# Kernel tuning notes

Measured on AMD Instinct MI355X. Metric: run time of the kernel, lower is better.

## Reference

```python
import jax, jax.numpy as jnp
import numpy as np
import math

B, C_IN, C_QK, H, W, NH = 1, 256, 128, 96, 96, 8
SCALE = math.sqrt(C_QK / NH)  # sqrt(planes/num_head) = 4.0
TEMP = 1.0


def conv1x1(x, w, b=None):
    # x: [B, Cin, H, W], w: [Cout, Cin] -> [B, Cout, H, W]
    y = jnp.einsum('bchw,oc->bohw', x, w)
    if b is not None:
        y = y + b[None, :, None, None]
    return y


def maxpool2x2(x):
    return jax.lax.reduce_window(x, -jnp.inf, jax.lax.max,
                                 (1, 1, 2, 2), (1, 1, 2, 2), 'VALID')


def setup_inputs() -> dict:
    key = jax.random.key(0)
    ks = jax.random.split(key, 5)
    x = jax.random.normal(ks[0], (B, C_IN, H, W), dtype=jnp.float32)
    # conv weights: init.normal_(w, 0, 0.01), zero bias; conv_value has no bias
    w_q = jax.random.normal(ks[1], (C_QK, C_IN), dtype=jnp.float32) * 0.01
    b_q = jnp.zeros((C_QK,), dtype=jnp.float32)
    w_k = jax.random.normal(ks[2], (C_QK, C_IN), dtype=jnp.float32) * 0.01
    b_k = jnp.zeros((C_QK,), dtype=jnp.float32)
    w_v = jax.random.normal(ks[3], (C_IN, C_IN), dtype=jnp.float32) * 0.01
    return {'x': x, 'w_q': w_q, 'b_q': b_q, 'w_k': w_k, 'b_k': b_k, 'w_v': w_v}


def reference(x, w_q, b_q, w_k, b_k, w_v):
    residual = x
    input_x = maxpool2x2(x)                       # [B, Cin, H/2, W/2]
    Hd, Wd = H // 2, W // 2
    Nq, Nk = H * W, Hd * Wd

    q = conv1x1(x, w_q, b_q)                      # [B, Cqk, H, W]
    k = conv1x1(input_x, w_k, b_k)                # [B, Cqk, Hd, Wd]
    v = conv1x1(input_x, w_v)                     # [B, Cin, Hd, Wd]

    dq = C_QK // NH
    dv = C_IN // NH
    q = q.reshape(B * NH, dq, Nq)
    k = k.reshape(B * NH, dq, Nk)
    v = v.reshape(B * NH, dv, Nk)

    # dot distance: scaled by sqrt(planes/num_head) and temp (nowd empty)
    sim = jnp.einsum('bdq,bdk->bqk', q, k) / (SCALE * TEMP)
    attn = jax.nn.softmax(sim, axis=2)            # softmax over keys

    # out = value @ attn^T  -> [B*NH, dv, Nq]
    out = jnp.einsum('bdk,bqk->bdq', v, attn)
    out = out.reshape(B, C_IN, H, W)
    return out + residual
```

## Files before the change

### kernel.cpp

```cpp
#include <hip/hip_runtime.h>
#include <hip/hip_bf16.h>
#include <math.h>

#define C_IN   256
#define C_QK   128
#define NH     8
#define H_     96
#define W_     96
#define NQ     (H_*W_)
#define HD     48
#define WD     48
#define NK     (HD*WD)
#define DQ     16
#define DV     32
#define NQC    (NQ/32)
#define NKC    (NK/32)
#define QPAIRS (NQC/2)
#define KQRT   (NKC/4)
#define KSTEPS (C_IN/16)
#define QS     0.3606737602222409f

typedef __attribute__((ext_vector_type(8)))  short short8v;
typedef __attribute__((ext_vector_type(16))) float f32x16;
typedef __attribute__((ext_vector_type(2)))  int   v2i;

union B8u { uint u[4]; short8v v; };

static __device__ inline ushort bf16r(float f) {
    __hip_bfloat16 h = __float2bfloat16(f);
    return *reinterpret_cast<ushort*>(&h);
}
static __device__ inline uint cvtpk(float lo, float hi) {
    uint r;
    asm("v_cvt_pk_bf16_f32 %0, %1, %2" : "=v"(r) : "v"(lo), "v"(hi));
    return r;
}
static __device__ inline void lswap(uint a, uint b, uint& x, uint& y, int hi) {
#if __has_builtin(__builtin_amdgcn_permlane32_swap)
    v2i r = __builtin_amdgcn_permlane32_swap((int)a, (int)b, false, false);
    x = (uint)r.x;
    y = (uint)r.y;
#else
    uint bx = (uint)__shfl_xor((int)b, 32);
    uint ax = (uint)__shfl_xor((int)a, 32);
    x = hi ? bx : a;
    y = hi ? b : ax;
#endif
}
static __device__ inline float fexp2(float v) {
#if __has_builtin(__builtin_amdgcn_exp2f)
    return __builtin_amdgcn_exp2f(v);
#else
    return __expf(v * 0.6931471805599453f);
#endif
}

#define U_XPB  (NKC*KSTEPS*64)
#define U_WQ   (4*KSTEPS*64)
#define U_WK   (4*KSTEPS*64)
#define U_WV   (8*KSTEPS*64)
#define U_FRAG (U_XPB+U_WQ+U_WK+U_WV)
#define U_TOT  (U_FRAG + 128)

__global__ __launch_bounds__(256) void prep_kernel(
    const float* __restrict__ x,  const float* __restrict__ wq, const float* __restrict__ bq,
    const float* __restrict__ wk, const float* __restrict__ wv,
    ushort* __restrict__ xpbP,
    ushort* __restrict__ wqP, ushort* __restrict__ wkP, ushort* __restrict__ wvP,
    float* __restrict__ bqs)
{
    int t = blockIdx.x * 256 + threadIdx.x;
    if (t >= U_TOT) return;
    if (t >= U_FRAG) { int i = t - U_FRAG; bqs[i] = bq[i] * QS; return; }

    union { ushort s[8]; uint4 v; } ou;
    int u = t;
    if (u < U_XPB) {
        int l = u & 63, rest = u >> 6;
        int ks = rest & 15, nc = rest >> 4;
        int np = nc * 32 + (l & 31);
        int k0 = ks * 16 + 8 * (l >> 5);
        int py = np / WD, px = np - py * WD;
        const float* base = x + (2 * py) * W_ + 2 * px;
        #pragma unroll
        for (int j = 0; j < 8; ++j) {
            const float* p = base + (size_t)(k0 + j) * NQ;
            ou.s[j] = bf16r(fmaxf(fmaxf(p[0], p[1]), fmaxf(p[W_], p[W_ + 1])));
        }
        *(uint4*)&xpbP[(size_t)u * 8] = ou.v;
        return;
    }
    u -= U_XPB;
    if (u < U_WQ) {
        int l = u & 63, ks = (u >> 6) & 15, mb = u >> 10;
        int m = mb * 32 + (l & 31), k0 = ks * 16 + 8 * (l >> 5);
        #pragma unroll
        for (int j = 0; j < 8; ++j) ou.s[j] = bf16r(wq[m * C_IN + k0 + j] * QS);
        *(uint4*)&wqP[(size_t)u * 8] = ou.v;
        return;
    }
    u -= U_WQ;
    if (u < U_WK) {
        int l = u & 63, ks = (u >> 6) & 15, mb = u >> 10;
        int m = mb * 32 + (l & 31), k0 = ks * 16 + 8 * (l >> 5);
        #pragma unroll
        for (int j = 0; j < 8; ++j) ou.s[j] = bf16r(wk[m * C_IN + k0 + j]);
        *(uint4*)&wkP[(size_t)u * 8] = ou.v;
        return;
    }
    u -= U_WK;
    {
        int l = u & 63, ks = (u >> 6) & 15, cb = u >> 10;
        int c = cb * 32 + (l & 31), k0 = ks * 16 + 8 * (l >> 5);
        #pragma unroll
        for (int j = 0; j < 8; ++j) ou.s[j] = bf16r(wv[c * C_IN + k0 + j]);
        *(uint4*)&wvP[(size_t)u * 8] = ou.v;
    }
}

static __device__ inline f32x16 mfma_loop(const ushort* __restrict__ A,
                                          const ushort* __restrict__ B) {
    f32x16 acc;
    #pragma unroll
    for (int r = 0; r < 16; ++r) acc[r] = 0.0f;
    #pragma unroll
    for (int s = 0; s < KSTEPS; ++s) {
        short8v a = *(const short8v*)(A + (size_t)s * 512);
        short8v b = *(const short8v*)(B + (size_t)s * 512);
        acc = __builtin_amdgcn_mfma_f32_32x32x16_bf16(a, b, acc, 0, 0, 0);
    }
    return acc;
}
static __device__ inline void xform(const f32x16& acc, int hi, short8v& F1, short8v& F2) {
    uint a0 = cvtpk(acc[0],  acc[1]),  a1 = cvtpk(acc[2],  acc[3]);
    uint b0 = cvtpk(acc[4],  acc[5]),  b1 = cvtpk(acc[6],  acc[7]);
    uint a2 = cvtpk(acc[8],  acc[9]),  a3 = cvtpk(acc[10], acc[11]);
    uint b2 = cvtpk(acc[12], acc[13]), b3 = cvtpk(acc[14], acc[15]);
    B8u f1, f2;
    lswap(a0, b0, f1.u[0], f1.u[2], hi);
    lswap(a1, b1, f1.u[1], f1.u[3], hi);
    lswap(a2, b2, f2.u[0], f2.u[2], hi);
    lswap(a3, b3, f2.u[1], f2.u[3], hi);
    F1 = f1.v; F2 = f2.v;
}

#define T_Q 1152
#define T_K (T_Q + 288)
#define T_ALL (T_K + 576)

__global__ __launch_bounds__(256) void gemm_fused(
    const float* __restrict__ x, const ushort* __restrict__ xpbP,
    const ushort* __restrict__ wqP, const ushort* __restrict__ wkP,
    const ushort* __restrict__ wvP,
    const float* __restrict__ bqs, const float* __restrict__ bk,
    ushort* __restrict__ qpack, ushort* __restrict__ kpack, ushort* __restrict__ vpack)
{
    int lane = threadIdx.x & 63, wvi = threadIdx.x >> 6;
    int hi = lane >> 5;
    int t = blockIdx.x * 4 + wvi;
    if (t >= T_ALL) return;

    if (t < T_Q) {
        int mb = t / NQC, nc = t - mb * NQC;
        const ushort* A = wqP + ((size_t)(mb * KSTEPS) * 64 + lane) * 8;
        const float* xb = x + (size_t)(8 * hi) * NQ + nc * 32 + (lane & 31);
        f32x16 acc;
        #pragma unroll
        for (int r = 0; r < 16; ++r) acc[r] = 0.0f;
        #pragma unroll
        for (int s = 0; s < KSTEPS; ++s) {
            float f[8];
            #pragma unroll
            for (int j = 0; j < 8; ++j) f[j] = xb[(size_t)(s * 16 + j) * NQ];
            B8u bf;
            #pragma unroll
            for (int m = 0; m < 4; ++m) bf.u[m] = cvtpk(f[2 * m], f[2 * m + 1]);
            short8v a = *(const short8v*)(A + (size_t)s * 512);
            acc = __builtin_amdgcn_mfma_f32_32x32x16_bf16(a, bf.v, acc, 0, 0, 0);
        }
        #pragma unroll
        for (int r = 0; r < 16; ++r)
            acc[r] += bqs[mb * 32 + (r & 3) + 8 * (r >> 2) + 4 * hi];
        short8v F1, F2;
        xform(acc, hi, F1, F2);
        *(short8v*)&qpack[((size_t)((2 * mb)     * NQC + nc) * 64 + lane) * 8] = F1;
        *(short8v*)&qpack[((size_t)((2 * mb + 1) * NQC + nc) * 64 + lane) * 8] = F2;
    } else if (t < T_K) {
        int t2 = t - T_Q;
        int mb = t2 / NKC, nc = t2 - mb * NKC;
        const ushort* A = wkP  + ((size_t)(mb * KSTEPS) * 64 + lane) * 8;
        const ushort* B = xpbP + ((size_t)(nc * KSTEPS) * 64 + lane) * 8;
        f32x16 acc = mfma_loop(A, B);
        #pragma unroll
        for (int r = 0; r < 16; ++r)
            acc[r] += bk[mb * 32 + (r & 3) + 8 * (r >> 2) + 4 * hi];
        short8v F1, F2;
        xform(acc, hi, F1, F2);
        *(short8v*)&kpack[((size_t)((2 * mb)     * NKC + nc) * 64 + lane) * 8] = F1;
        *(short8v*)&kpack[((size_t)((2 * mb + 1) * NKC + nc) * 64 + lane) * 8] = F2;
    } else {
        int t3 = t - T_K;
        int cb = t3 / NKC, kc = t3 - cb * NKC;
        const ushort* A = xpbP + ((size_t)(kc * KSTEPS) * 64 + lane) * 8;
        const ushort* B = wvP  + ((size_t)(cb * KSTEPS) * 64 + lane) * 8;
        f32x16 acc = mfma_loop(A, B);
        short8v F1, F2;
        xform(acc, hi, F1, F2);
        *(short8v*)&vpack[((size_t)((cb * NKC + kc) * 2 + 0) * 64 + lane) * 8] = F1;
        *(short8v*)&vpack[((size_t)((cb * NKC + kc) * 2 + 1) * 64 + lane) * 8] = F2;
    }
}

static __device__ inline void qstep(short8v kcur, short8v qf, short8v v0c, short8v v1c,
                                    f32x16& o, float& rs, const f32x16& zc, int hi) {
    f32x16 s = __builtin_amdgcn_mfma_f32_32x32x16_bf16(kcur, qf, zc, 0, 0, 0);
    {
        float e0 = fexp2(s[0]), e1 = fexp2(s[1]), e2 = fexp2(s[2]), e3 = fexp2(s[3]);
        float e4 = fexp2(s[4]), e5 = fexp2(s[5]), e6 = fexp2(s[6]), e7 = fexp2(s[7]);
        rs += ((e0 + e1) + (e2 + e3)) + ((e4 + e5) + (e6 + e7));
        uint a0 = cvtpk(e0, e1), a1 = cvtpk(e2, e3);
        uint b0 = cvtpk(e4, e5), b1 = cvtpk(e6, e7);
        B8u B1;
        lswap(a0, b0, B1.u[0], B1.u[2], hi);
        lswap(a1, b1, B1.u[1], B1.u[3], hi);
        o = __builtin_amdgcn_mfma_f32_32x32x16_bf16(v0c, B1.v, o, 0, 0, 0);
    }
    {
        float e0 = fexp2(s[8]),  e1 = fexp2(s[9]),  e2 = fexp2(s[10]), e3 = fexp2(s[11]);
        float e4 = fexp2(s[12]), e5 = fexp2(s[13]), e6 = fexp2(s[14]), e7 = fexp2(s[15]);
        rs += ((e0 + e1) + (e2 + e3)) + ((e4 + e5) + (e6 + e7));
        uint a0 = cvtpk(e0, e1), a1 = cvtpk(e2, e3);
        uint b0 = cvtpk(e4, e5), b1 = cvtpk(e6, e7);
        B8u B2;
        lswap(a0, b0, B2.u[0], B2.u[2], hi);
        lswap(a1, b1, B2.u[1], B2.u[3], hi);
        o = __builtin_amdgcn_mfma_f32_32x32x16_bf16(v1c, B2.v, o, 0, 0, 0);
    }
}

__global__ __launch_bounds__(256) void attn_kernel(const ushort* __restrict__ qpack,
                                                   const ushort* __restrict__ kpack,
                                                   const ushort* __restrict__ vpack,
                                                   const float* __restrict__ x,
                                                   float* __restrict__ out) {
    __shared__ float part[4][2][64][20];
    const int h = blockIdx.y;
    const int tid = threadIdx.x, lane = tid & 63;
    const int kh = tid >> 6;
    const int q31 = lane & 31, hi = lane >> 5;
    const int qp = blockIdx.x;

    short8v qf0 = *(const short8v*)&qpack[((size_t)(h * NQC + 2 * qp)     * 64 + lane) * 8];
    short8v qf1 = *(const short8v*)&qpack[((size_t)(h * NQC + 2 * qp + 1) * 64 + lane) * 8];

    const ushort* kp = kpack + ((size_t)(h * NKC + kh * KQRT) * 64 + lane) * 8;
    const ushort* vp = vpack + ((size_t)(h * NKC + kh * KQRT) * 2 * 64 + lane) * 8;

    short8v kf = *(const short8v*)kp;
    short8v v0 = *(const short8v*)vp;

    f32x16 o0, o1, zc;
    #pragma unroll
    for (int r = 0; r < 16; ++r) { o0[r] = 0.0f; o1[r] = 0.0f; zc[r] = 0.0f; }
    float rs0 = 0.0f, rs1 = 0.0f;

    for (int c = 0; c < KQRT; ++c) {
        short8v kcur = kf, v0c = v0;
        short8v v1c = *(const short8v*)(vp + (size_t)c * 1024 + 512);
        int cn = (c == KQRT - 1) ? 0 : (c + 1);
        kf = *(const short8v*)(kp + (size_t)cn * 512);
        v0 = *(const short8v*)(vp + (size_t)cn * 1024);

        qstep(kcur, qf0, v0c, v1c, o0, rs0, zc, hi);
        qstep(kcur, qf1, v0c, v1c, o1, rs1, zc, hi);
    }

    rs0 += __shfl_xor(rs0, 32);
    rs1 += __shfl_xor(rs1, 32);

    {
        float* p0 = &part[kh][0][lane][0];
        #pragma unroll
        for (int i = 0; i < 4; ++i)
            *(float4*)&p0[4 * i] = *(float4*)((const float*)&o0 + 4 * i);
        p0[16] = rs0;
        float* p1 = &part[kh][1][lane][0];
        #pragma unroll
        for (int i = 0; i < 4; ++i)
            *(float4*)&p1[4 * i] = *(float4*)((const float*)&o1 + 4 * i);
        p1[16] = rs1;
    }
    __syncthreads();

    if (kh < 2) {
        float o[16] = {};
        float rs = 0.0f;
        #pragma unroll
        for (int w = 0; w < 4; ++w) {
            const float* pw = &part[w][kh][lane][0];
            #pragma unroll
            for (int i = 0; i < 4; ++i) {
                float4 f = *(const float4*)&pw[4 * i];
                o[4 * i + 0] += f.x; o[4 * i + 1] += f.y;
                o[4 * i + 2] += f.z; o[4 * i + 3] += f.w;
            }
            rs += pw[16];
        }
        float inv = 1.0f / rs;
        int q = (2 * qp + kh) * 32 + q31;
        #pragma unroll
        for (int r = 0; r < 16; ++r) {
            int dv = (r & 3) + 8 * (r >> 2) + 4 * hi;
            size_t i0 = (size_t)(h * DV + dv) * NQ + q;
            out[i0] = o[r] * inv + x[i0];
        }
    }
}

extern "C" void kernel_launch(void* const* d_in, const int* in_sizes, int n_in,
                              void* d_out, int out_size, void* d_ws, size_t ws_size,
                              hipStream_t stream) {
    const float* x  = (const float*)d_in[0];
    const float* wq = (const float*)d_in[1];
    const float* bq = (const float*)d_in[2];
    const float* wk = (const float*)d_in[3];
    const float* bk = (const float*)d_in[4];
    const float* wv = (const float*)d_in[5];
    float* out = (float*)d_out;

    ushort* p = (ushort*)d_ws;
    ushort* xpbP  = p;  p += (size_t)U_XPB * 8;
    ushort* wqP   = p;  p += (size_t)U_WQ  * 8;
    ushort* wkP   = p;  p += (size_t)U_WK  * 8;
    ushort* wvP   = p;  p += (size_t)U_WV  * 8;
    ushort* qpack = p;  p += (size_t)NH * NQC * 64 * 8;
    ushort* kpack = p;  p += (size_t)NH * NKC * 64 * 8;
    ushort* vpack = p;  p += (size_t)NH * NKC * 2 * 64 * 8;
    float*  bqs   = (float*)p;

    prep_kernel<<<(U_TOT + 255) / 256, 256, 0, stream>>>(x, wq, bq, wk, wv,
                                                         xpbP, wqP, wkP, wvP, bqs);
    gemm_fused<<<(T_ALL + 3) / 4, 256, 0, stream>>>(x, xpbP, wqP, wkP, wvP,
                                                    bqs, bk, qpack, kpack, vpack);
    attn_kernel<<<dim3(QPAIRS, NH), 256, 0, stream>>>(qpack, kpack, vpack, x, out);
}
```

Measured before the change: 116.5 us.

## Prepack x to bf16 fragments in prep and split attention to one q-chunk per block

The prep kernel now also converts full-resolution x into bf16 MFMA fragment layout, so the Q projection in the GEMM kernel uses the shared mfma_loop instead of strided fp32 loads with in-loop conversion. The attention kernel now gives each block a single 32-query chunk instead of two, doubling the grid. The final reduction across the four key-split waves is spread over all four waves, each writing four output rows, with a padded LDS stride. This trades an extra bf16 copy of x, more blocks and duplicated K/V loads for better occupancy and less per-block serial work.

```diff
diff --git a/kernel.cpp b/kernel.cpp
--- a/kernel.cpp
+++ b/kernel.cpp
@@ -15,7 +15,6 @@
 #define DV     32
 #define NQC    (NQ/32)
 #define NKC    (NK/32)
-#define QPAIRS (NQC/2)
 #define KQRT   (NKC/4)
 #define KSTEPS (C_IN/16)
 #define QS     0.3606737602222409f
@@ -55,17 +54,18 @@
 #endif
 }
 
+#define U_XB   (NQC*KSTEPS*64)
 #define U_XPB  (NKC*KSTEPS*64)
 #define U_WQ   (4*KSTEPS*64)
 #define U_WK   (4*KSTEPS*64)
 #define U_WV   (8*KSTEPS*64)
-#define U_FRAG (U_XPB+U_WQ+U_WK+U_WV)
+#define U_FRAG (U_XB+U_XPB+U_WQ+U_WK+U_WV)
 #define U_TOT  (U_FRAG + 128)
 
 __global__ __launch_bounds__(256) void prep_kernel(
     const float* __restrict__ x,  const float* __restrict__ wq, const float* __restrict__ bq,
     const float* __restrict__ wk, const float* __restrict__ wv,
-    ushort* __restrict__ xpbP,
+    ushort* __restrict__ xbP, ushort* __restrict__ xpbP,
     ushort* __restrict__ wqP, ushort* __restrict__ wkP, ushort* __restrict__ wvP,
     float* __restrict__ bqs)
 {
@@ -75,6 +75,17 @@
 
     union { ushort s[8]; uint4 v; } ou;
     int u = t;
+    if (u < U_XB) {
+        int l = u & 63, rest = u >> 6;
+        int ks = rest & 15, nc = rest >> 4;
+        int n  = nc * 32 + (l & 31);
+        int k0 = ks * 16 + 8 * (l >> 5);
+        #pragma unroll
+        for (int j = 0; j < 8; ++j) ou.s[j] = bf16r(x[(size_t)(k0 + j) * NQ + n]);
+        *(uint4*)&xbP[(size_t)u * 8] = ou.v;
+        return;
+    }
+    u -= U_XB;
     if (u < U_XPB) {
         int l = u & 63, rest = u >> 6;
         int ks = rest & 15, nc = rest >> 4;
@@ -149,7 +160,7 @@
 #define T_ALL (T_K + 576)
 
 __global__ __launch_bounds__(256) void gemm_fused(
-    const float* __restrict__ x, const ushort* __restrict__ xpbP,
+    const ushort* __restrict__ xbP, const ushort* __restrict__ xpbP,
     const ushort* __restrict__ wqP, const ushort* __restrict__ wkP,
     const ushort* __restrict__ wvP,
     const float* __restrict__ bqs, const float* __restrict__ bk,
@@ -163,21 +174,8 @@
     if (t < T_Q) {
         int mb = t / NQC, nc = t - mb * NQC;
         const ushort* A = wqP + ((size_t)(mb * KSTEPS) * 64 + lane) * 8;
-        const float* xb = x + (size_t)(8 * hi) * NQ + nc * 32 + (lane & 31);
-        f32x16 acc;
-        #pragma unroll
-        for (int r = 0; r < 16; ++r) acc[r] = 0.0f;
-        #pragma unroll
-        for (int s = 0; s < KSTEPS; ++s) {
-            float f[8];
-            #pragma unroll
-            for (int j = 0; j < 8; ++j) f[j] = xb[(size_t)(s * 16 + j) * NQ];
-            B8u bf;
-            #pragma unroll
-            for (int m = 0; m < 4; ++m) bf.u[m] = cvtpk(f[2 * m], f[2 * m + 1]);
-            short8v a = *(const short8v*)(A + (size_t)s * 512);
-            acc = __builtin_amdgcn_mfma_f32_32x32x16_bf16(a, bf.v, acc, 0, 0, 0);
-        }
+        const ushort* B = xbP + ((size_t)(nc * KSTEPS) * 64 + lane) * 8;
+        f32x16 acc = mfma_loop(A, B);
         #pragma unroll
         for (int r = 0; r < 16; ++r)
             acc[r] += bqs[mb * 32 + (r & 3) + 8 * (r >> 2) + 4 * hi];
@@ -211,47 +209,20 @@
     }
 }
 
-static __device__ inline void qstep(short8v kcur, short8v qf, short8v v0c, short8v v1c,
-                                    f32x16& o, float& rs, const f32x16& zc, int hi) {
-    f32x16 s = __builtin_amdgcn_mfma_f32_32x32x16_bf16(kcur, qf, zc, 0, 0, 0);
-    {
-        float e0 = fexp2(s[0]), e1 = fexp2(s[1]), e2 = fexp2(s[2]), e3 = fexp2(s[3]);
-        float e4 = fexp2(s[4]), e5 = fexp2(s[5]), e6 = fexp2(s[6]), e7 = fexp2(s[7]);
-        rs += ((e0 + e1) + (e2 + e3)) + ((e4 + e5) + (e6 + e7));
-        uint a0 = cvtpk(e0, e1), a1 = cvtpk(e2, e3);
-        uint b0 = cvtpk(e4, e5), b1 = cvtpk(e6, e7);
-        B8u B1;
-        lswap(a0, b0, B1.u[0], B1.u[2], hi);
-        lswap(a1, b1, B1.u[1], B1.u[3], hi);
-        o = __builtin_amdgcn_mfma_f32_32x32x16_bf16(v0c, B1.v, o, 0, 0, 0);
-    }
-    {
-        float e0 = fexp2(s[8]),  e1 = fexp2(s[9]),  e2 = fexp2(s[10]), e3 = fexp2(s[11]);
-        float e4 = fexp2(s[12]), e5 = fexp2(s[13]), e6 = fexp2(s[14]), e7 = fexp2(s[15]);
-        rs += ((e0 + e1) + (e2 + e3)) + ((e4 + e5) + (e6 + e7));
-        uint a0 = cvtpk(e0, e1), a1 = cvtpk(e2, e3);
-        uint b0 = cvtpk(e4, e5), b1 = cvtpk(e6, e7);
-        B8u B2;
-        lswap(a0, b0, B2.u[0], B2.u[2], hi);
-        lswap(a1, b1, B2.u[1], B2.u[3], hi);
-        o = __builtin_amdgcn_mfma_f32_32x32x16_bf16(v1c, B2.v, o, 0, 0, 0);
-    }
-}
+#define CSTR 17
 
 __global__ __launch_bounds__(256) void attn_kernel(const ushort* __restrict__ qpack,
                                                    const ushort* __restrict__ kpack,
                                                    const ushort* __restrict__ vpack,
                                                    const float* __restrict__ x,
                                                    float* __restrict__ out) {
-    __shared__ float part[4][2][64][20];
-    const int h = blockIdx.y;
+    __shared__ float part[4][64][CSTR];
+    const int h = blockIdx.y, qc = blockIdx.x;
     const int tid = threadIdx.x, lane = tid & 63;
     const int kh = tid >> 6;
     const int q31 = lane & 31, hi = lane >> 5;
-    const int qp = blockIdx.x;
-
-    short8v qf0 = *(const short8v*)&qpack[((size_t)(h * NQC + 2 * qp)     * 64 + lane) * 8];
-    short8v qf1 = *(const short8v*)&qpack[((size_t)(h * NQC + 2 * qp + 1) * 64 + lane) * 8];
+
+    short8v qf = *(const short8v*)&qpack[((size_t)(h * NQC + qc) * 64 + lane) * 8];
 
     const ushort* kp = kpack + ((size_t)(h * NKC + kh * KQRT) * 64 + lane) * 8;
     const ushort* vp = vpack + ((size_t)(h * NKC + kh * KQRT) * 2 * 64 + lane) * 8;
@@ -259,10 +230,10 @@
     short8v kf = *(const short8v*)kp;
     short8v v0 = *(const short8v*)vp;
 
-    f32x16 o0, o1, zc;
+    f32x16 o, zc;
     #pragma unroll
-    for (int r = 0; r < 16; ++r) { o0[r] = 0.0f; o1[r] = 0.0f; zc[r] = 0.0f; }
-    float rs0 = 0.0f, rs1 = 0.0f;
+    for (int r = 0; r < 16; ++r) { o[r] = 0.0f; zc[r] = 0.0f; }
+    float rs = 0.0f;
 
     for (int c = 0; c < KQRT; ++c) {
         short8v kcur = kf, v0c = v0;
@@ -271,49 +242,53 @@
         kf = *(const short8v*)(kp + (size_t)cn * 512);
         v0 = *(const short8v*)(vp + (size_t)cn * 1024);
 
-        qstep(kcur, qf0, v0c, v1c, o0, rs0, zc, hi);
-        qstep(kcur, qf1, v0c, v1c, o1, rs1, zc, hi);
-    }
-
-    rs0 += __shfl_xor(rs0, 32);
-    rs1 += __shfl_xor(rs1, 32);
+        f32x16 s = __builtin_amdgcn_mfma_f32_32x32x16_bf16(kcur, qf, zc, 0, 0, 0);
+        {
+            float e0 = fexp2(s[0]), e1 = fexp2(s[1]), e2 = fexp2(s[2]), e3 = fexp2(s[3]);
+            float e4 = fexp2(s[4]), e5 = fexp2(s[5]), e6 = fexp2(s[6]), e7 = fexp2(s[7]);
+            rs += ((e0 + e1) + (e2 + e3)) + ((e4 + e5) + (e6 + e7));
+            uint a0 = cvtpk(e0, e1), a1 = cvtpk(e2, e3);
+            uint b0 = cvtpk(e4, e5), b1 = cvtpk(e6, e7);
+            B8u B1;
+            lswap(a0, b0, B1.u[0], B1.u[2], hi);
+            lswap(a1, b1, B1.u[1], B1.u[3], hi);
+            o = __builtin_amdgcn_mfma_f32_32x32x16_bf16(v0c, B1.v, o, 0, 0, 0);
+        }
+        {
+            float e0 = fexp2(s[8]),  e1 = fexp2(s[9]),  e2 = fexp2(s[10]), e3 = fexp2(s[11]);
+            float e4 = fexp2(s[12]), e5 = fexp2(s[13]), e6 = fexp2(s[14]), e7 = fexp2(s[15]);
+            rs += ((e0 + e1) + (e2 + e3)) + ((e4 + e5) + (e6 + e7));
+            uint a0 = cvtpk(e0, e1), a1 = cvtpk(e2, e3);
+            uint b0 = cvtpk(e4, e5), b1 = cvtpk(e6, e7);
+            B8u B2;
+            lswap(a0, b0, B2.u[0], B2.u[2], hi);
+            lswap(a1, b1, B2.u[1], B2.u[3], hi);
+            o = __builtin_amdgcn_mfma_f32_32x32x16_bf16(v1c, B2.v, o, 0, 0, 0);
+        }
+    }
+
+    rs += __shfl_xor(rs, 32);
 
     {
-        float* p0 = &part[kh][0][lane][0];
-        #pragma unroll
-        for (int i = 0; i < 4; ++i)
-            *(float4*)&p0[4 * i] = *(float4*)((const float*)&o0 + 4 * i);
-        p0[16] = rs0;
-        float* p1 = &part[kh][1][lane][0];
-        #pragma unroll
-        for (int i = 0; i < 4; ++i)
-            *(float4*)&p1[4 * i] = *(float4*)((const float*)&o1 + 4 * i);
-        p1[16] = rs1;
+        float* pw = &part[kh][lane][0];
+        #pragma unroll
+        for (int r = 0; r < 16; ++r) pw[r] = o[r];
+        pw[16] = rs;
     }
     __syncthreads();
 
-    if (kh < 2) {
-        float o[16] = {};
-        float rs = 0.0f;
-        #pragma unroll
-        for (int w = 0; w < 4; ++w) {
-            const float* pw = &part[w][kh][lane][0];
-            #pragma unroll
-            for (int i = 0; i < 4; ++i) {
-                float4 f = *(const float4*)&pw[4 * i];
-                o[4 * i + 0] += f.x; o[4 * i + 1] += f.y;
-                o[4 * i + 2] += f.z; o[4 * i + 3] += f.w;
-            }
-            rs += pw[16];
-        }
-        float inv = 1.0f / rs;
-        int q = (2 * qp + kh) * 32 + q31;
-        #pragma unroll
-        for (int r = 0; r < 16; ++r) {
-            int dv = (r & 3) + 8 * (r >> 2) + 4 * hi;
-            size_t i0 = (size_t)(h * DV + dv) * NQ + q;
-            out[i0] = o[r] * inv + x[i0];
-        }
+    float rsAll = part[0][lane][16] + part[1][lane][16]
+                + part[2][lane][16] + part[3][lane][16];
+    float inv = 1.0f / rsAll;
+    int q = qc * 32 + q31;
+    #pragma unroll
+    for (int i = 0; i < 4; ++i) {
+        int r = 4 * kh + i;
+        float val = part[0][lane][r] + part[1][lane][r]
+                  + part[2][lane][r] + part[3][lane][r];
+        int dv = i + 8 * kh + 4 * hi;
+        size_t i0 = (size_t)(h * DV + dv) * NQ + q;
+        out[i0] = val * inv + x[i0];
     }
 }
 
@@ -329,6 +304,7 @@
     float* out = (float*)d_out;
 
     ushort* p = (ushort*)d_ws;
+    ushort* xbP   = p;  p += (size_t)U_XB  * 8;
     ushort* xpbP  = p;  p += (size_t)U_XPB * 8;
     ushort* wqP   = p;  p += (size_t)U_WQ  * 8;
     ushort* wkP   = p;  p += (size_t)U_WK  * 8;
@@ -339,8 +315,8 @@
     float*  bqs   = (float*)p;
 
     prep_kernel<<<(U_TOT + 255) / 256, 256, 0, stream>>>(x, wq, bq, wk, wv,
-                                                         xpbP, wqP, wkP, wvP, bqs);
-    gemm_fused<<<(T_ALL + 3) / 4, 256, 0, stream>>>(x, xpbP, wqP, wkP, wvP,
+                                                         xbP, xpbP, wqP, wkP, wvP, bqs);
+    gemm_fused<<<(T_ALL + 3) / 4, 256, 0, stream>>>(xbP, xpbP, wqP, wkP, wvP,
                                                     bqs, bk, qpack, kpack, vpack);
-    attn_kernel<<<dim3(QPAIRS, NH), 256, 0, stream>>>(qpack, kpack, vpack, x, out);
-}
+    attn_kernel<<<dim3(NQC, NH), 256, 0, stream>>>(qpack, kpack, vpack, x, out);
+}
```

Result: no change. 114.6 us (-1.6%).
